# Kernel optimization log

Measured on AMD Instinct MI355X. Metric: run time of the kernel, lower is better.

Reference implementation:

```python
import jax, jax.numpy as jnp
import numpy as np

N = 50000      # nodes
E = 800000     # edges per sampled adjacency
F_IN = 128     # input features
H = 256        # hidden
C = 112        # classes (ogbn-proteins)
L = 8          # num_layers
EPS = 1e-5     # BatchNorm eps


def setup_inputs() -> dict:
    key = jax.random.key(0)
    ks = jax.random.split(key, 8)
    x = jax.random.normal(ks[0], (N, F_IN), dtype=jnp.float32)
    edge1 = jax.random.randint(ks[1], (2, E), 0, N)
    edge2 = jax.random.randint(ks[2], (2, E), 0, N)
    in_W = jax.random.normal(ks[3], (F_IN, H), dtype=jnp.float32) * 0.05
    in_b = jnp.zeros((H,), jnp.float32)
    convW = jax.random.normal(ks[4], (L, H, H), dtype=jnp.float32) * 0.05
    convB = jnp.zeros((L, H), jnp.float32)
    bn_gamma = jnp.ones((L, H), jnp.float32)
    bn_beta = jnp.zeros((L, H), jnp.float32)
    out_W = jax.random.normal(ks[5], (H, C), dtype=jnp.float32) * 0.05
    out_b = jnp.zeros((C,), jnp.float32)
    layer_w = jax.random.normal(ks[6], (L,), dtype=jnp.float32)
    return dict(x=x, edge1=edge1, edge2=edge2, in_W=in_W, in_b=in_b,
                convW=convW, convB=convB, bn_gamma=bn_gamma, bn_beta=bn_beta,
                out_W=out_W, out_b=out_b, layer_w=layer_w)


def _gcn_norm(edge_index):
    # GCNConv default: add self-loops, sym-normalize D^{-1/2} A_hat D^{-1/2}.
    loops = jnp.arange(N)
    row = jnp.concatenate([edge_index[0], loops])  # source
    col = jnp.concatenate([edge_index[1], loops])  # target
    deg = jax.ops.segment_sum(jnp.ones_like(row, jnp.float32), col, num_segments=N)
    dinv = jnp.where(deg > 0, jax.lax.rsqrt(deg), 0.0)
    return row, col, dinv[row] * dinv[col]


def reference(x, edge1, edge2, in_W, in_b, convW, convB, bn_gamma, bn_beta,
              out_W, out_b, layer_w):
    adj1 = _gcn_norm(edge1)
    adj2 = _gcn_norm(edge2)
    h = x @ in_W + in_b                                  # input_fc: [N, H]
    w = jax.nn.softmax(layer_w)                          # residual layer weights
    acc = jnp.zeros_like(h)
    for i in range(L):
        row, col, norm = adj1 if i < L // 2 else adj2
        t = h @ convW[i] + convB[i]                      # GCNConv linear
        msg = t[row] * norm[:, None]                     # gather + scale  [E+N, H]
        h = jax.ops.segment_sum(msg, col, num_segments=N)  # scatter-add SpMM
        mu = h.mean(axis=0)                              # BatchNorm1d (batch stats)
        var = h.var(axis=0)
        h = (h - mu) * jax.lax.rsqrt(var + EPS) * bn_gamma[i] + bn_beta[i]
        h = jax.nn.relu(h)                               # dropout is identity in eval
        acc = acc + w[i] * h                             # weighted residual sum
    out = acc @ out_W + out_b                            # out_fc: [N, C]
    return jax.nn.log_softmax(out, axis=1)
```

## Files before the change

### kernel.cpp

```cpp
#include <hip/hip_runtime.h>
#include <math.h>

#define NN 50000
#define HH 256
#define FIN 128
#define CC 112
#define LL 8
#define EE 800000
#define EPSB 1e-5f

typedef unsigned short u16;
typedef unsigned int u32;
typedef __attribute__((ext_vector_type(8))) short bf16x8;
typedef __attribute__((ext_vector_type(4))) float f32x4;

__device__ __forceinline__ u16 f2bf(float f) {
    u32 u = __float_as_uint(f);
    u32 r = (u + 0x7FFFu + ((u >> 16) & 1u)) >> 16;
    return (u16)r;
}
__device__ __forceinline__ float bflo(u32 u) { return __uint_as_float(u << 16); }
__device__ __forceinline__ float bfhi(u32 u) { return __uint_as_float(u & 0xFFFF0000u); }
__device__ __forceinline__ float bf1(u16 u) { return __uint_as_float(((u32)u) << 16); }

__device__ __forceinline__ void gload16(const u16* g, u16* l) {
    __builtin_amdgcn_global_load_lds(
        (const __attribute__((address_space(1))) void*)g,
        (__attribute__((address_space(3))) void*)l, 16, 0, 0);
}

__global__ void k_fill2(const int* __restrict__ ed1, const int* __restrict__ ed2,
                        int* __restrict__ cur, int* __restrict__ src1p,
                        int* __restrict__ src2p) {
    int e = blockIdx.x * blockDim.x + threadIdx.x;
    if (e >= 2 * EE) return;
    const int* ed = (e < EE) ? ed1 : ed2;
    int* sp = (e < EE) ? src1p : src2p;
    int* cu = (e < EE) ? cur : cur + NN;
    int ee = (e < EE) ? e : e - EE;
    int r = ed[ee];
    int c = ed[ee + EE];
    int pos = atomicAdd(&cu[c], 1);
    sp[(c << 6) + pos] = r;
}

__global__ void k_dinv2(const int* __restrict__ deg, float* __restrict__ dinv1,
                        float* __restrict__ dinv2, int n) {
    int v = blockIdx.x * blockDim.x + threadIdx.x;
    if (v >= 2 * n) return;
    float* d = (v < n) ? dinv1 : dinv2;
    int vv = (v < n) ? v : v - n;
    d[vv] = rsqrtf((float)(deg[v] + 1));
}

__global__ void k_wt(const float* __restrict__ W, u16* __restrict__ Wt, int K, int N) {
    __shared__ u16 sm[32][33];
    const float* Wl = W + (size_t)blockIdx.z * K * N;
    u16* Wtl = Wt + (size_t)blockIdx.z * K * N;
    int k0 = blockIdx.y * 32, n0 = blockIdx.x * 32;
    int tx = threadIdx.x, ty = threadIdx.y;
#pragma unroll
    for (int r = 0; r < 32; r += 8)
        sm[ty + r][tx] = f2bf(Wl[(size_t)(k0 + ty + r) * N + n0 + tx]);
    __syncthreads();
#pragma unroll
    for (int r = 0; r < 32; r += 8)
        Wtl[(size_t)(n0 + ty + r) * K + k0 + tx] = sm[tx][ty + r];
}

__global__ void k_outwt(const float* __restrict__ outW, const float* __restrict__ outb,
                        u16* __restrict__ outWt, float* __restrict__ obb) {
    int idx = blockIdx.x * 256 + threadIdx.x;
    if (idx >= 128 * 256) return;
    int n = idx >> 8, k = idx & 255;
    float v = (n < CC) ? outW[(size_t)k * CC + n] : 0.f;
    outWt[(size_t)n * HH + k] = f2bf(v);
    if (idx < 128) obb[idx] = (idx < CC) ? outb[idx] : 0.f;
}

__global__ void k_xcast(const float* __restrict__ x, u16* __restrict__ xb, int n4) {
    int i = blockIdx.x * blockDim.x + threadIdx.x;
    if (i >= n4) return;
    float4 v = ((const float4*)x)[i];
    ushort4 o;
    o.x = f2bf(v.x); o.y = f2bf(v.y); o.z = f2bf(v.z); o.w = f2bf(v.w);
    *(ushort4*)(xb + ((size_t)i << 2)) = o;
}

template <bool F32OUT, bool SWIZ>
__global__ __launch_bounds__(256) void k_gemm_bf16(const u16* __restrict__ A,
                                                   const u16* __restrict__ Bt,
                                                   const float* __restrict__ bias,
                                                   const float* __restrict__ rowscale,
                                                   void* __restrict__ Cout,
                                                   int M, int Nc, int K) {
    int m0, n0;
    if (SWIZ) {
        int id = blockIdx.x;
        int g = id >> 4, r = id & 15;
        int m = g * 8 + (r & 7);
        if (m * 128 >= M) return;
        m0 = m * 128;
        n0 = (r >> 3) * 128;
    } else {
        m0 = blockIdx.x * 128;
        n0 = 0;
    }
    __shared__ u16 As[128 * 32];
    __shared__ u16 Bs[128 * 32];
    const int tid = threadIdx.x;
    const int w = tid >> 6, lane = tid & 63;
    const int wr = (w >> 1) * 64, wc = (w & 1) * 64;
    const int lm = lane & 15, lq = lane >> 4;

    f32x4 acc[4][4];
#pragma unroll
    for (int i = 0; i < 4; ++i)
#pragma unroll
        for (int j = 0; j < 4; ++j) acc[i][j] = (f32x4){0.f, 0.f, 0.f, 0.f};

    const int srow = w * 16 + (lane >> 2);
    const int scol = (lane & 3) * 8;

    for (int k0 = 0; k0 < K; k0 += 32) {
        int gm = m0 + srow;        if (gm >= M) gm = M - 1;
        gload16(A + (size_t)gm * K + k0 + scol, As + (size_t)(w * 64) * 8);
        int gm2 = m0 + 64 + srow;  if (gm2 >= M) gm2 = M - 1;
        gload16(A + (size_t)gm2 * K + k0 + scol, As + (size_t)(256 + w * 64) * 8);
        gload16(Bt + (size_t)(n0 + srow) * K + k0 + scol, Bs + (size_t)(w * 64) * 8);
        gload16(Bt + (size_t)(n0 + 64 + srow) * K + k0 + scol, Bs + (size_t)(256 + w * 64) * 8);
        __syncthreads();

        bf16x8 af[4], bfr[4];
#pragma unroll
        for (int i = 0; i < 4; ++i)
            af[i] = *(const bf16x8*)(As + (wr + i * 16 + lm) * 32 + lq * 8);
#pragma unroll
        for (int j = 0; j < 4; ++j)
            bfr[j] = *(const bf16x8*)(Bs + (wc + j * 16 + lm) * 32 + lq * 8);
#pragma unroll
        for (int i = 0; i < 4; ++i)
#pragma unroll
            for (int j = 0; j < 4; ++j)
                acc[i][j] = __builtin_amdgcn_mfma_f32_16x16x32_bf16(af[i], bfr[j], acc[i][j], 0, 0, 0);
        __syncthreads();
    }

#pragma unroll
    for (int j = 0; j < 4; ++j) {
        int gc = n0 + wc + j * 16 + lm;
        float bj = (gc < Nc) ? bias[gc] : 0.f;
#pragma unroll
        for (int i = 0; i < 4; ++i) {
#pragma unroll
            for (int r = 0; r < 4; ++r) {
                int gr = m0 + wr + i * 16 + lq * 4 + r;
                if (gr < M && gc < Nc) {
                    float rs = rowscale ? rowscale[gr] : 1.0f;
                    float val = (acc[i][j][r] + bj) * rs;
                    if (F32OUT)
                        ((float*)Cout)[(size_t)gr * Nc + gc] = val;
                    else
                        ((u16*)Cout)[(size_t)gr * Nc + gc] = f2bf(val);
                }
            }
        }
    }
}

__global__ __launch_bounds__(512) void k_spmm_bf16(const u16* __restrict__ t,
                                                   const int* __restrict__ deg,
                                                   const int* __restrict__ srcp,
                                                   const float* __restrict__ dinv,
                                                   u16* __restrict__ hpre,
                                                   float* __restrict__ bns,
                                                   float* __restrict__ bnq) {
    __shared__ float lsum[8][HH];
    __shared__ float lsq[8][HH];
    int w = threadIdx.x >> 6;
    int lane = threadIdx.x & 63;
    int c = lane << 2;
    const u16* tp = t + c;
    float4 ssum = make_float4(0.f, 0.f, 0.f, 0.f);
    float4 ssq  = make_float4(0.f, 0.f, 0.f, 0.f);
    int vbase = (blockIdx.x * 8 + w) * 2;

    for (int i = 0; i < 2; ++i) {
        int v = vbase + i;
        const int* src = srcp + (v << 6);
        float dv = dinv[v];
        uint2 a = *(const uint2*)(tp + (size_t)v * HH);
        float4 accv;
        accv.x = bflo(a.x); accv.y = bfhi(a.x);
        accv.z = bflo(a.y); accv.w = bfhi(a.y);
        int end = deg[v];
        int j = 0;
        for (; j + 8 <= end; j += 8) {
            int4 sA = *(const int4*)(src + j);
            int4 sB = *(const int4*)(src + j + 4);
            uint2 b0 = *(const uint2*)(tp + (size_t)sA.x * HH);
            uint2 b1 = *(const uint2*)(tp + (size_t)sA.y * HH);
            uint2 b2 = *(const uint2*)(tp + (size_t)sA.z * HH);
            uint2 b3 = *(const uint2*)(tp + (size_t)sA.w * HH);
            uint2 b4 = *(const uint2*)(tp + (size_t)sB.x * HH);
            uint2 b5 = *(const uint2*)(tp + (size_t)sB.y * HH);
            uint2 b6 = *(const uint2*)(tp + (size_t)sB.z * HH);
            uint2 b7 = *(const uint2*)(tp + (size_t)sB.w * HH);
            accv.x += bflo(b0.x) + bflo(b1.x) + bflo(b2.x) + bflo(b3.x)
                    + bflo(b4.x) + bflo(b5.x) + bflo(b6.x) + bflo(b7.x);
            accv.y += bfhi(b0.x) + bfhi(b1.x) + bfhi(b2.x) + bfhi(b3.x)
                    + bfhi(b4.x) + bfhi(b5.x) + bfhi(b6.x) + bfhi(b7.x);
            accv.z += bflo(b0.y) + bflo(b1.y) + bflo(b2.y) + bflo(b3.y)
                    + bflo(b4.y) + bflo(b5.y) + bflo(b6.y) + bflo(b7.y);
            accv.w += bfhi(b0.y) + bfhi(b1.y) + bfhi(b2.y) + bfhi(b3.y)
                    + bfhi(b4.y) + bfhi(b5.y) + bfhi(b6.y) + bfhi(b7.y);
        }
        for (; j + 2 <= end; j += 2) {
            int s0 = src[j], s1 = src[j + 1];
            uint2 b0 = *(const uint2*)(tp + (size_t)s0 * HH);
            uint2 b1 = *(const uint2*)(tp + (size_t)s1 * HH);
            accv.x += bflo(b0.x) + bflo(b1.x);
            accv.y += bfhi(b0.x) + bfhi(b1.x);
            accv.z += bflo(b0.y) + bflo(b1.y);
            accv.w += bfhi(b0.y) + bfhi(b1.y);
        }
        if (j < end) {
            int s0 = src[j];
            uint2 b0 = *(const uint2*)(tp + (size_t)s0 * HH);
            accv.x += bflo(b0.x); accv.y += bfhi(b0.x);
            accv.z += bflo(b0.y); accv.w += bfhi(b0.y);
        }
        ushort4 o;
        o.x = f2bf(accv.x * dv); o.y = f2bf(accv.y * dv);
        o.z = f2bf(accv.z * dv); o.w = f2bf(accv.w * dv);
        *(ushort4*)(hpre + (size_t)v * HH + c) = o;

        float vx = bf1(o.x), vy = bf1(o.y), vz = bf1(o.z), vw = bf1(o.w);
        ssum.x += vx; ssum.y += vy; ssum.z += vz; ssum.w += vw;
        ssq.x = fmaf(vx, vx, ssq.x); ssq.y = fmaf(vy, vy, ssq.y);
        ssq.z = fmaf(vz, vz, ssq.z); ssq.w = fmaf(vw, vw, ssq.w);
    }

    lsum[w][c + 0] = ssum.x; lsum[w][c + 1] = ssum.y;
    lsum[w][c + 2] = ssum.z; lsum[w][c + 3] = ssum.w;
    lsq[w][c + 0] = ssq.x; lsq[w][c + 1] = ssq.y;
    lsq[w][c + 2] = ssq.z; lsq[w][c + 3] = ssq.w;
    __syncthreads();
    int tid = threadIdx.x;
    if (tid < HH) {
        float s = 0.f;
#pragma unroll
        for (int ww = 0; ww < 8; ++ww) s += lsum[ww][tid];
        atomicAdd(&bns[(blockIdx.x & 7) * HH + tid], s);
    } else {
        int tcol = tid - HH;
        float q = 0.f;
#pragma unroll
        for (int ww = 0; ww < 8; ++ww) q += lsq[ww][tcol];
        atomicAdd(&bnq[(blockIdx.x & 7) * HH + tcol], q);
    }
}

__global__ __launch_bounds__(256) void k_bnnorm(const u16* __restrict__ hpre,
                         u16* __restrict__ accb, u16* __restrict__ hb,
                         const float* __restrict__ bins,
                         const float* __restrict__ gamma, const float* __restrict__ beta,
                         const float* __restrict__ wArr, int layer) {
    __shared__ float sscale[HH], sshift[HH];
    const float invN = 1.0f / (float)NN;
    {
        int tcol = threadIdx.x;
        float m = 0.f, qq = 0.f;
#pragma unroll
        for (int b = 0; b < 8; ++b) {
            m += bins[b * HH + tcol];
            qq += bins[(8 + b) * HH + tcol];
        }
        m *= invN;
        float var = qq * invN - m * m;
        float sc = rsqrtf(var + EPSB) * gamma[tcol];
        sscale[tcol] = sc;
        sshift[tcol] = beta[tcol] - m * sc;
    }
    __syncthreads();
    int idx = blockIdx.x * blockDim.x + threadIdx.x;
    if (idx >= NN * (HH / 4)) return;
    int c = (idx & 63) << 2;
    float w = wArr[layer];
    ushort4 hv = ((const ushort4*)hpre)[idx];
    ushort4 av = ((const ushort4*)accb)[idx];
    u16* hp = &hv.x;
    u16* ap = &av.x;
    ushort4 oh, oa;
    u16* ohp = &oh.x;
    u16* oap = &oa.x;
#pragma unroll
    for (int k = 0; k < 4; ++k) {
        float v = fmaf(bf1(hp[k]), sscale[c + k], sshift[c + k]);
        v = fmaxf(v, 0.f);
        oap[k] = f2bf(fmaf(w, v, bf1(ap[k])));
        ohp[k] = f2bf(v);
    }
    ((ushort4*)accb)[idx] = oa;
    *(ushort4*)(hb + ((size_t)idx << 2)) = oh;
}

__global__ void k_softmaxw(const float* __restrict__ lw, float* __restrict__ wArr) {
    if (threadIdx.x == 0 && blockIdx.x == 0) {
        float m = -3.0e38f;
        for (int i = 0; i < LL; ++i) m = fmaxf(m, lw[i]);
        float e[LL]; float sum = 0.f;
        for (int i = 0; i < LL; ++i) { e[i] = expf(lw[i] - m); sum += e[i]; }
        for (int i = 0; i < LL; ++i) wArr[i] = e[i] / sum;
    }
}

__global__ __launch_bounds__(256) void k_logsoftmax(const float* __restrict__ z,
                                                    float* __restrict__ out) {
    int gt = blockIdx.x * blockDim.x + threadIdx.x;
    int v = gt >> 6;
    int lane = threadIdx.x & 63;
    if (v >= NN) return;
    const float* row = z + (size_t)v * CC;
    float v0 = row[lane];
    float v1 = (lane + 64 < CC) ? row[lane + 64] : -3.0e38f;
    float m = fmaxf(v0, v1);
#pragma unroll
    for (int d = 1; d < 64; d <<= 1) m = fmaxf(m, __shfl_xor(m, d, 64));
    float e = expf(v0 - m) + ((lane + 64 < CC) ? expf(v1 - m) : 0.f);
#pragma unroll
    for (int d = 1; d < 64; d <<= 1) e += __shfl_xor(e, d, 64);
    float lse = m + logf(e);
    out[(size_t)v * CC + lane] = v0 - lse;
    if (lane + 64 < CC) out[(size_t)v * CC + lane + 64] = v1 - lse;
}

extern "C" void kernel_launch(void* const* d_in, const int* in_sizes, int n_in,
                              void* d_out, int out_size, void* d_ws, size_t ws_size,
                              hipStream_t stream) {
    const float* x     = (const float*)d_in[0];
    const int*   e1    = (const int*)d_in[1];
    const int*   e2    = (const int*)d_in[2];
    const float* inW   = (const float*)d_in[3];
    const float* inb   = (const float*)d_in[4];
    const float* convW = (const float*)d_in[5];
    const float* convB = (const float*)d_in[6];
    const float* gamma = (const float*)d_in[7];
    const float* beta  = (const float*)d_in[8];
    const float* outW  = (const float*)d_in[9];
    const float* outb  = (const float*)d_in[10];
    const float* lw    = (const float*)d_in[11];

    char* ws = (char*)d_ws;
    size_t off = 0;
    auto alloc = [&](size_t bytes) -> void* {
        void* p = ws + off;
        off = (off + bytes + 255) & ~(size_t)255;
        return p;
    };
    u16*   hb    = (u16*)alloc((size_t)NN * HH * 2);
    u16*   tb    = (u16*)alloc((size_t)NN * HH * 2);
    u16*   hpre  = (u16*)alloc((size_t)NN * HH * 2);
    u16*   accb  = (u16*)alloc((size_t)NN * HH * 2);
    u16*   convWt= (u16*)alloc((size_t)LL * HH * HH * 2);
    u16*   inWt  = (u16*)alloc((size_t)HH * FIN * 2);
    u16*   outWt = (u16*)alloc((size_t)128 * HH * 2);
    float* obb   = (float*)alloc(128 * 4);
    float* dinv1 = (float*)alloc((size_t)NN * 4);
    float* dinv2 = (float*)alloc((size_t)NN * 4);
    int*   src1p = (int*)alloc((size_t)NN * 64 * 4);
    int*   src2p = (int*)alloc((size_t)NN * 64 * 4);
    int*   curz  = (int*)alloc((size_t)2 * NN * 4);
    float* bnsq  = (float*)alloc((size_t)LL * 16 * HH * 4);
    float* wArr  = (float*)alloc(64);
    u16*   xb    = tb;
    float* logits = (float*)hpre;

    int* cur1 = curz;

    const int NB = (NN + 255) / 256;

    hipMemsetAsync(curz, 0, (size_t)2 * NN * 4, stream);
    hipMemsetAsync(bnsq, 0, (size_t)LL * 16 * HH * 4, stream);
    hipMemsetAsync(accb, 0, (size_t)NN * HH * 2, stream);

    k_fill2<<<(2 * EE + 255) / 256, 256, 0, stream>>>(e1, e2, curz, src1p, src2p);
    k_dinv2<<<(2 * NN + 255) / 256, 256, 0, stream>>>(curz, dinv1, dinv2, NN);

    k_softmaxw<<<1, 64, 0, stream>>>(lw, wArr);

    {
        dim3 g(HH / 32, HH / 32, LL);
        dim3 b(32, 8);
        k_wt<<<g, b, 0, stream>>>(convW, convWt, HH, HH);
        dim3 g2(HH / 32, FIN / 32, 1);
        k_wt<<<g2, b, 0, stream>>>(inW, inWt, FIN, HH);
        k_outwt<<<128, 256, 0, stream>>>(outW, outb, outWt, obb);
    }
    k_xcast<<<(NN * FIN / 4 + 255) / 256, 256, 0, stream>>>(x, xb, NN * FIN / 4);

    const int MT = (NN + 127) / 128;
    const int GSW = ((MT + 7) / 8) * 16;
    k_gemm_bf16<false, true><<<GSW, 256, 0, stream>>>(xb, inWt, inb, nullptr, hb, NN, HH, FIN);

    const int SPB = NN / 16;
    const int ELB = (NN * (HH / 4) + 255) / 256;
    for (int i = 0; i < LL; ++i) {
        const int* dg = (i < LL / 2) ? cur1 : (curz + NN);
        const int* sr = (i < LL / 2) ? src1p : src2p;
        const float* dv = (i < LL / 2) ? dinv1 : dinv2;
        float* bins = bnsq + (size_t)i * 16 * HH;
        k_gemm_bf16<false, true><<<GSW, 256, 0, stream>>>(hb, convWt + (size_t)i * HH * HH,
                                                          convB + (size_t)i * HH, dv, tb,
                                                          NN, HH, HH);
        k_spmm_bf16<<<SPB, 512, 0, stream>>>(tb, dg, sr, dv, hpre,
                                             bins, bins + 8 * HH);
        k_bnnorm<<<ELB, 256, 0, stream>>>(hpre, accb, hb, bins,
                                          gamma + (size_t)i * HH, beta + (size_t)i * HH,
                                          wArr, i);
    }

    k_gemm_bf16<true, false><<<MT, 256, 0, stream>>>(accb, outWt, obb, nullptr, logits,
                                                     NN, CC, HH);
    k_logsoftmax<<<NN / 4, 256, 0, stream>>>(logits, (float*)d_out);
}
```

Before: 1.227 ms.

## Store CSR source indices as u16 and partition edge fill by destination group

Neighbor source indices are stored as 16-bit values, which is valid because N fits in 16 bits. This halves the index storage and the index loads in the SpMM inner loop, where eight indices now come from one 16-byte load. The edge-fill kernel is restructured so each of 8 block groups, selected by blockIdx modulo 8, handles only destinations in its node range. The intent is to keep atomics and scattered writes local to one cache partition. In exchange, every group scans the full edge lists, so edge reads increase eightfold.

```diff
diff --git a/kernel.cpp b/kernel.cpp
--- a/kernel.cpp
+++ b/kernel.cpp
@@ -8,6 +8,8 @@
 #define LL 8
 #define EE 800000
 #define EPSB 1e-5f
+#define NGRP 8
+#define NPG (NN / NGRP)
 
 typedef unsigned short u16;
 typedef unsigned int u32;
@@ -29,19 +31,31 @@
         (__attribute__((address_space(3))) void*)l, 16, 0, 0);
 }
 
-__global__ void k_fill2(const int* __restrict__ ed1, const int* __restrict__ ed2,
-                        int* __restrict__ cur, int* __restrict__ src1p,
-                        int* __restrict__ src2p) {
-    int e = blockIdx.x * blockDim.x + threadIdx.x;
-    if (e >= 2 * EE) return;
-    const int* ed = (e < EE) ? ed1 : ed2;
-    int* sp = (e < EE) ? src1p : src2p;
-    int* cu = (e < EE) ? cur : cur + NN;
-    int ee = (e < EE) ? e : e - EE;
-    int r = ed[ee];
-    int c = ed[ee + EE];
-    int pos = atomicAdd(&cu[c], 1);
-    sp[(c << 6) + pos] = r;
+__global__ __launch_bounds__(256) void k_fill2(const int* __restrict__ ed1,
+                                               const int* __restrict__ ed2,
+                                               int* __restrict__ cur,
+                                               u16* __restrict__ src1p,
+                                               u16* __restrict__ src2p) {
+    const int g = blockIdx.x & 7;
+    const int bg = blockIdx.x >> 3;
+    const int nthr = (gridDim.x >> 3) * 256;
+    const int tid = bg * 256 + threadIdx.x;
+    const int lo = g * NPG;
+
+    for (int e = tid; e < EE; e += nthr) {
+        int c = ed1[e + EE];
+        if ((u32)(c - lo) < (u32)NPG) {
+            int pos = atomicAdd(&cur[c], 1);
+            src1p[(c << 6) + pos] = (u16)ed1[e];
+        }
+    }
+    for (int e = tid; e < EE; e += nthr) {
+        int c = ed2[e + EE];
+        if ((u32)(c - lo) < (u32)NPG) {
+            int pos = atomicAdd(&cur[NN + c], 1);
+            src2p[(c << 6) + pos] = (u16)ed2[e];
+        }
+    }
 }
 
 __global__ void k_dinv2(const int* __restrict__ deg, float* __restrict__ dinv1,
@@ -170,7 +184,7 @@
 
 __global__ __launch_bounds__(512) void k_spmm_bf16(const u16* __restrict__ t,
                                                    const int* __restrict__ deg,
-                                                   const int* __restrict__ srcp,
+                                                   const u16* __restrict__ srcp,
                                                    const float* __restrict__ dinv,
                                                    u16* __restrict__ hpre,
                                                    float* __restrict__ bns,
@@ -187,7 +201,7 @@
 
     for (int i = 0; i < 2; ++i) {
         int v = vbase + i;
-        const int* src = srcp + (v << 6);
+        const u16* src = srcp + (v << 6);
         float dv = dinv[v];
         uint2 a = *(const uint2*)(tp + (size_t)v * HH);
         float4 accv;
@@ -196,16 +210,19 @@
         int end = deg[v];
         int j = 0;
         for (; j + 8 <= end; j += 8) {
-            int4 sA = *(const int4*)(src + j);
-            int4 sB = *(const int4*)(src + j + 4);
-            uint2 b0 = *(const uint2*)(tp + (size_t)sA.x * HH);
-            uint2 b1 = *(const uint2*)(tp + (size_t)sA.y * HH);
-            uint2 b2 = *(const uint2*)(tp + (size_t)sA.z * HH);
-            uint2 b3 = *(const uint2*)(tp + (size_t)sA.w * HH);
-            uint2 b4 = *(const uint2*)(tp + (size_t)sB.x * HH);
-            uint2 b5 = *(const uint2*)(tp + (size_t)sB.y * HH);
-            uint2 b6 = *(const uint2*)(tp + (size_t)sB.z * HH);
-            uint2 b7 = *(const uint2*)(tp + (size_t)sB.w * HH);
+            uint4 sp = *(const uint4*)(src + j);
+            int s0 = sp.x & 0xFFFF, s1 = sp.x >> 16;
+            int s2 = sp.y & 0xFFFF, s3 = sp.y >> 16;
+            int s4 = sp.z & 0xFFFF, s5 = sp.z >> 16;
+            int s6 = sp.w & 0xFFFF, s7 = sp.w >> 16;
+            uint2 b0 = *(const uint2*)(tp + (size_t)s0 * HH);
+            uint2 b1 = *(const uint2*)(tp + (size_t)s1 * HH);
+            uint2 b2 = *(const uint2*)(tp + (size_t)s2 * HH);
+            uint2 b3 = *(const uint2*)(tp + (size_t)s3 * HH);
+            uint2 b4 = *(const uint2*)(tp + (size_t)s4 * HH);
+            uint2 b5 = *(const uint2*)(tp + (size_t)s5 * HH);
+            uint2 b6 = *(const uint2*)(tp + (size_t)s6 * HH);
+            uint2 b7 = *(const uint2*)(tp + (size_t)s7 * HH);
             accv.x += bflo(b0.x) + bflo(b1.x) + bflo(b2.x) + bflo(b3.x)
                     + bflo(b4.x) + bflo(b5.x) + bflo(b6.x) + bflo(b7.x);
             accv.y += bfhi(b0.x) + bfhi(b1.x) + bfhi(b2.x) + bfhi(b3.x)
@@ -368,8 +385,8 @@
     float* obb   = (float*)alloc(128 * 4);
     float* dinv1 = (float*)alloc((size_t)NN * 4);
     float* dinv2 = (float*)alloc((size_t)NN * 4);
-    int*   src1p = (int*)alloc((size_t)NN * 64 * 4);
-    int*   src2p = (int*)alloc((size_t)NN * 64 * 4);
+    u16*   src1p = (u16*)alloc((size_t)NN * 64 * 2);
+    u16*   src2p = (u16*)alloc((size_t)NN * 64 * 2);
     int*   curz  = (int*)alloc((size_t)2 * NN * 4);
     float* bnsq  = (float*)alloc((size_t)LL * 16 * HH * 4);
     float* wArr  = (float*)alloc(64);
@@ -378,13 +395,11 @@
 
     int* cur1 = curz;
 
-    const int NB = (NN + 255) / 256;
-
     hipMemsetAsync(curz, 0, (size_t)2 * NN * 4, stream);
     hipMemsetAsync(bnsq, 0, (size_t)LL * 16 * HH * 4, stream);
     hipMemsetAsync(accb, 0, (size_t)NN * HH * 2, stream);
 
-    k_fill2<<<(2 * EE + 255) / 256, 256, 0, stream>>>(e1, e2, curz, src1p, src2p);
+    k_fill2<<<8 * 256, 256, 0, stream>>>(e1, e2, curz, src1p, src2p);
     k_dinv2<<<(2 * NN + 255) / 256, 256, 0, stream>>>(curz, dinv1, dinv2, NN);
 
     k_softmaxw<<<1, 64, 0, stream>>>(lw, wArr);
@@ -407,7 +422,7 @@
     const int ELB = (NN * (HH / 4) + 255) / 256;
     for (int i = 0; i < LL; ++i) {
         const int* dg = (i < LL / 2) ? cur1 : (curz + NN);
-        const int* sr = (i < LL / 2) ? src1p : src2p;
+        const u16* sr = (i < LL / 2) ? src1p : src2p;
         const float* dv = (i < LL / 2) ? dinv1 : dinv2;
         float* bins = bnsq + (size_t)i * 16 * HH;
         k_gemm_bf16<false, true><<<GSW, 256, 0, stream>>>(hb, convWt + (size_t)i * HH * HH,
```

Result: faster. 1.187 ms (-3.3%).
